# Kernel optimization log

Measured on AMD Instinct MI355X. Metric: run time of the kernel, lower is better.

## Reference

```python
import jax, jax.numpy as jnp
import numpy as np

NUM_HEADS = 16
HEAD_DIM = 64
HIDDEN = NUM_HEADS * HEAD_DIM
LN_EPS = 1e-6


def setup_inputs() -> dict:
    key = jax.random.key(0)
    ks = jax.random.split(key, 5)
    B, T, H = 2, 2048, HIDDEN
    s = 1.0 / np.sqrt(H)
    return {
        "h": jax.random.normal(ks[0], (B, T, H), jnp.float32),
        "Wq": jax.random.normal(ks[1], (H, H), jnp.float32) * s,
        "bq": jnp.zeros((H,), jnp.float32),
        "Wk": jax.random.normal(ks[2], (H, H), jnp.float32) * s,
        "bk": jnp.zeros((H,), jnp.float32),
        "Wv": jax.random.normal(ks[3], (H, H), jnp.float32) * s,
        "bv": jnp.zeros((H,), jnp.float32),
        "Wo": jax.random.normal(ks[4], (H, H), jnp.float32) * s,
        "bo": jnp.zeros((H,), jnp.float32),
        "gamma": jnp.ones((H,), jnp.float32),
        "beta": jnp.zeros((H,), jnp.float32),
    }


def _split_heads(x):
    B, T, H = x.shape
    return x.reshape(B, T, NUM_HEADS, HEAD_DIM).transpose(0, 2, 1, 3)  # [B,h,T,d]


def reference(h, Wq, bq, Wk, bk, Wv, bv, Wo, bo, gamma, beta):
    # QKV projections (nn.Linear: x @ W^T + b)
    Q = _split_heads(h @ Wq.T + bq)
    K = _split_heads(h @ Wk.T + bk)
    V = _split_heads(h @ Wv.T + bv)
    scale = HEAD_DIM ** -0.5
    scores = jnp.einsum("bhqd,bhkd->bhqk", Q, K) * scale  # [B,h,T,T]
    attn = jax.nn.softmax(scores, axis=-1)
    ctx = jnp.einsum("bhqk,bhkd->bhqd", attn, V)          # [B,h,T,d]
    B, _, T, _ = ctx.shape
    ctx = ctx.transpose(0, 2, 1, 3).reshape(B, T, HIDDEN)
    out = ctx @ Wo.T + bo + h  # dropout is identity at eval
    # LayerNorm(eps=1e-6)
    mu = out.mean(-1, keepdims=True)
    var = jnp.mean((out - mu) ** 2, -1, keepdims=True)
    return (out - mu) * jax.lax.rsqrt(var + LN_EPS) * gamma + beta
```

## Files before the change

kernel.cpp:

```cpp
#include <hip/hip_runtime.h>
#include <hip/hip_bf16.h>

#define NH   16
#define HD   64
#define HID  1024
#define TSEQ 2048
#define BATCH 2
#define KSCALE 0.18033688011112042f

typedef __attribute__((ext_vector_type(4))) float f32x4;
typedef __attribute__((ext_vector_type(8))) short s16x8;
typedef __attribute__((ext_vector_type(4))) short s16x4;
typedef __attribute__((ext_vector_type(8))) _Float16 f16x8;
typedef __attribute__((ext_vector_type(4))) _Float16 f16x4;

__device__ __forceinline__ unsigned short f2bf(float f) {
  union { float f; unsigned int u; } v; v.f = f;
  unsigned int r = v.u + 0x7fffu + ((v.u >> 16) & 1u);
  return (unsigned short)(r >> 16);
}
__device__ __forceinline__ float bf2f(unsigned short b) {
  union { unsigned int u; float f; } v; v.u = ((unsigned int)b) << 16; return v.f;
}

__device__ __forceinline__ void async_cp16(const unsigned short* g, unsigned short* l) {
  __builtin_amdgcn_global_load_lds(
      (const __attribute__((address_space(1))) unsigned int*)g,
      (__attribute__((address_space(3))) unsigned int*)l, 16, 0, 0);
}

__global__ __launch_bounds__(256) void cast_all_k(
    const float* __restrict__ h,
    const float* __restrict__ w0, const float* __restrict__ w1,
    const float* __restrict__ w2, const float* __restrict__ w3,
    unsigned short* __restrict__ hb, unsigned short* __restrict__ wbase) {
  int i = blockIdx.x * 256 + threadIdx.x;
  const float* src; unsigned short* dst; int idx; float sc = 1.f;
  if (i < 1048576) { src = h; dst = hb; idx = i; }
  else {
    int idx4 = i - 1048576;
    int w = idx4 >> 18;
    idx = idx4 & 262143;
    src = (w == 0) ? w0 : (w == 1) ? w1 : (w == 2) ? w2 : w3;
    dst = wbase + (size_t)(idx4 - idx) * 4;
    if (w == 1) sc = KSCALE;
  }
  float4 v = ((const float4*)src)[idx];
  ushort4 o;
  o.x = f2bf(v.x * sc); o.y = f2bf(v.y * sc); o.z = f2bf(v.z * sc); o.w = f2bf(v.w * sc);
  ((ushort4*)dst)[idx] = o;
}

__device__ __forceinline__ void gemm_core(const unsigned short* __restrict__ Ag,
                                          const unsigned short* __restrict__ Bg,
                                          unsigned short* Ash, unsigned short* Bsh,
                                          f32x4 acc[4][4]) {
  const int tid  = threadIdx.x;
  const int lane = tid & 63;
  const int wave = tid >> 6;
  const int l15  = lane & 15;
  const int quad = lane >> 4;
  const int wm   = (wave >> 1) * 64;
  const int wn   = (wave & 1) * 64;
  const int idx0 = tid * 8;
  const int idx1 = idx0 + 2048;
  const int r0 = idx0 >> 5, c0 = idx0 & 31;
  const int r1 = idx1 >> 5, c1 = idx1 & 31;
#pragma unroll
  for (int i = 0; i < 4; ++i)
#pragma unroll
    for (int j = 0; j < 4; ++j) acc[i][j] = f32x4{0.f, 0.f, 0.f, 0.f};

  for (int k0 = 0; k0 < HID; k0 += 32) {
    __syncthreads();
    async_cp16(Ag + r0 * HID + k0 + c0, Ash + idx0);
    async_cp16(Ag + r1 * HID + k0 + c1, Ash + idx1);
    async_cp16(Bg + r0 * HID + k0 + c0, Bsh + idx0);
    async_cp16(Bg + r1 * HID + k0 + c1, Bsh + idx1);
    __syncthreads();
    s16x8 af[4], bfr[4];
#pragma unroll
    for (int i = 0; i < 4; ++i)
      af[i] = *(const s16x8*)(Ash + (wm + i * 16 + l15) * 32 + quad * 8);
#pragma unroll
    for (int j = 0; j < 4; ++j)
      bfr[j] = *(const s16x8*)(Bsh + (wn + j * 16 + l15) * 32 + quad * 8);
#pragma unroll
    for (int i = 0; i < 4; ++i)
#pragma unroll
      for (int j = 0; j < 4; ++j)
        acc[i][j] = __builtin_amdgcn_mfma_f32_16x16x32_bf16(af[i], bfr[j], acc[i][j], 0, 0, 0);
  }
}

__global__ __launch_bounds__(256) void gemm_qkv(
    const unsigned short* __restrict__ hb,
    const unsigned short* __restrict__ wq, const unsigned short* __restrict__ wk,
    const unsigned short* __restrict__ wv,
    const float* __restrict__ bq, const float* __restrict__ bk, const float* __restrict__ bv,
    unsigned short* __restrict__ qo, unsigned short* __restrict__ ko,
    unsigned short* __restrict__ vto) {
  __shared__ unsigned short Ash[128 * 32];
  __shared__ unsigned short Bsh[128 * 32];
  const unsigned short* Bw; const float* bias; float bsc = 1.f;
  if (blockIdx.z == 0)      { Bw = wq; bias = bq; }
  else if (blockIdx.z == 1) { Bw = wk; bias = bk; bsc = KSCALE; }
  else                      { Bw = wv; bias = bv; }
  const int bm = blockIdx.y * 128, bn = blockIdx.x * 128;
  f32x4 acc[4][4];
  gemm_core(hb + (size_t)bm * HID, Bw + (size_t)bn * HID, Ash, Bsh, acc);

  const int tid = threadIdx.x, lane = tid & 63, wave = tid >> 6;
  const int l15 = lane & 15, quad = lane >> 4;
  const int wm = (wave >> 1) * 64, wn = (wave & 1) * 64;
  if (blockIdx.z == 2) {
#pragma unroll
    for (int j = 0; j < 4; ++j) {
      const int col = bn + wn + j * 16 + l15;
      const float bb = bias[col];
      const int head = col >> 6, d = col & 63;
#pragma unroll
      for (int i = 0; i < 4; ++i) {
        const int row0 = bm + wm + i * 16 + quad * 4;
        const int bI = row0 >> 11, t0 = row0 & 2047;
        unsigned short o[4];
#pragma unroll
        for (int r = 0; r < 4; ++r) {
          _Float16 hv = (_Float16)(acc[i][j][r] + bb);
          o[r] = __builtin_bit_cast(unsigned short, hv);
        }
        *(s16x4*)(vto + ((size_t)((bI * NH + head) * HD + d)) * TSEQ + t0) = *(const s16x4*)o;
      }
    }
  } else {
    unsigned short* outp = (blockIdx.z == 0) ? qo : ko;
#pragma unroll
    for (int j = 0; j < 4; ++j) {
      const int col = bn + wn + j * 16 + l15;
      const float bb = bias[col] * bsc;
      const int head = col >> 6, d = col & 63;
#pragma unroll
      for (int i = 0; i < 4; ++i) {
#pragma unroll
        for (int r = 0; r < 4; ++r) {
          const int row = bm + wm + i * 16 + quad * 4 + r;
          const int bI = row >> 11, t = row & 2047;
          outp[(((size_t)(bI * NH + head) * TSEQ) + t) * HD + d] = f2bf(acc[i][j][r] + bb);
        }
      }
    }
  }
}

__global__ __launch_bounds__(256) void gemm_out(
    const unsigned short* __restrict__ ctx, const unsigned short* __restrict__ wo,
    const float* __restrict__ bo, const float* __restrict__ hres,
    float* __restrict__ outf) {
  __shared__ unsigned short Ash[128 * 32];
  __shared__ unsigned short Bsh[64 * 32];
  const int tid = threadIdx.x, lane = tid & 63, wave = tid >> 6;
  const int l15 = lane & 15, quad = lane >> 4;
  const int wm = (wave >> 1) * 64, wn = (wave & 1) * 32;
  const int bm = blockIdx.y * 128, bn = blockIdx.x * 64;
  const unsigned short* Ag = ctx + (size_t)bm * HID;
  const unsigned short* Bg = wo + (size_t)bn * HID;
  const int idx0 = tid * 8, idx1 = idx0 + 2048;
  const int r0 = idx0 >> 5, c0 = idx0 & 31;
  const int r1 = idx1 >> 5, c1 = idx1 & 31;
  f32x4 acc[4][2];
#pragma unroll
  for (int i = 0; i < 4; ++i)
#pragma unroll
    for (int j = 0; j < 2; ++j) acc[i][j] = f32x4{0.f, 0.f, 0.f, 0.f};

  for (int k0 = 0; k0 < HID; k0 += 32) {
    __syncthreads();
    async_cp16(Ag + r0 * HID + k0 + c0, Ash + idx0);
    async_cp16(Ag + r1 * HID + k0 + c1, Ash + idx1);
    async_cp16(Bg + r0 * HID + k0 + c0, Bsh + idx0);
    __syncthreads();
    s16x8 af[4], bfr[2];
#pragma unroll
    for (int i = 0; i < 4; ++i)
      af[i] = *(const s16x8*)(Ash + (wm + i * 16 + l15) * 32 + quad * 8);
#pragma unroll
    for (int j = 0; j < 2; ++j)
      bfr[j] = *(const s16x8*)(Bsh + (wn + j * 16 + l15) * 32 + quad * 8);
#pragma unroll
    for (int i = 0; i < 4; ++i)
#pragma unroll
      for (int j = 0; j < 2; ++j)
        acc[i][j] = __builtin_amdgcn_mfma_f32_16x16x32_bf16(af[i], bfr[j], acc[i][j], 0, 0, 0);
  }
#pragma unroll
  for (int j = 0; j < 2; ++j) {
    const int col = bn + wn + j * 16 + l15;
    const float bb = bo[col];
#pragma unroll
    for (int i = 0; i < 4; ++i) {
#pragma unroll
      for (int r = 0; r < 4; ++r) {
        const int row = bm + wm + i * 16 + quad * 4 + r;
        const size_t off = (size_t)row * HID + col;
        outf[off] = acc[i][j][r] + bb + hres[off];
      }
    }
  }
}

__global__ __launch_bounds__(256, 2) void attn_k(
    const unsigned short* __restrict__ qb, const unsigned short* __restrict__ kb,
    const unsigned short* __restrict__ vt, unsigned short* __restrict__ ctx,
    unsigned short* __restrict__ Opart, float* __restrict__ rsumP,
    int split, int ntiles) {
  __shared__ unsigned short Ksh[64 * 72];
  __shared__ unsigned short Vsh[64 * 72];

  const int tid = threadIdx.x, lane = tid & 63, wave = tid >> 6;
  const int l15 = lane & 15, quad = lane >> 4;
  const int z = blockIdx.z;
  const int b = split ? (z >> 1) : z;
  const int half = split ? (z & 1) : 0;
  const int h = blockIdx.y, qt = blockIdx.x;
  const size_t ho = ((size_t)(b * NH + h)) * TSEQ * HD;
  const unsigned short* Qh = qb + ho;
  const unsigned short* Kh = kb + ho;
  const unsigned short* Vh = vt + ho;
  const int q0 = qt * 128 + wave * 32;
  const int kt0 = half * ntiles;

  s16x8 qf[2][2];
#pragma unroll
  for (int s = 0; s < 2; ++s)
#pragma unroll
    for (int ks = 0; ks < 2; ++ks)
      qf[s][ks] = *(const s16x8*)(Qh + (size_t)(q0 + s * 16 + l15) * HD + ks * 32 + quad * 8);

  f32x4 accO[4][2];
  float rsum[2];
#pragma unroll
  for (int n2 = 0; n2 < 4; ++n2)
#pragma unroll
    for (int s = 0; s < 2; ++s) accO[n2][s] = f32x4{0.f, 0.f, 0.f, 0.f};
  rsum[0] = rsum[1] = 0.f;

  const int sr = tid >> 3, sc = (tid & 7) * 8;
  s16x8 kreg[2], vreg[2];
#pragma unroll
  for (int hf = 0; hf < 2; ++hf) {
    kreg[hf] = *(const s16x8*)(Kh + (size_t)(kt0 * 64 + sr + hf * 32) * HD + sc);
    vreg[hf] = *(const s16x8*)(Vh + (size_t)(sr + hf * 32) * TSEQ + kt0 * 64 + sc);
  }

  for (int kt = 0; kt < ntiles; ++kt) {
    __syncthreads();
#pragma unroll
    for (int hf = 0; hf < 2; ++hf) {
      *(s16x8*)(Ksh + (sr + hf * 32) * 72 + sc) = kreg[hf];
      *(s16x8*)(Vsh + (sr + hf * 32) * 72 + sc) = vreg[hf];
    }
    __syncthreads();
    if (kt + 1 < ntiles) {
      const int k0n = (kt0 + kt + 1) * 64;
#pragma unroll
      for (int hf = 0; hf < 2; ++hf) {
        kreg[hf] = *(const s16x8*)(Kh + (size_t)(k0n + sr + hf * 32) * HD + sc);
        vreg[hf] = *(const s16x8*)(Vh + (size_t)(sr + hf * 32) * TSEQ + k0n + sc);
      }
    }

    f32x4 accS[2][4];
#pragma unroll
    for (int s = 0; s < 2; ++s)
#pragma unroll
      for (int n = 0; n < 4; ++n) accS[s][n] = f32x4{0.f, 0.f, 0.f, 0.f};
#pragma unroll
    for (int ks = 0; ks < 2; ++ks) {
#pragma unroll
      for (int n = 0; n < 4; ++n) {
        s16x8 kf = *(const s16x8*)(Ksh + (n * 16 + l15) * 72 + ks * 32 + quad * 8);
#pragma unroll
        for (int s = 0; s < 2; ++s)
          accS[s][n] = __builtin_amdgcn_mfma_f32_16x16x32_bf16(kf, qf[s][ks], accS[s][n], 0, 0, 0);
      }
    }

    f16x4 pB[2][4];
#pragma unroll
    for (int s = 0; s < 2; ++s)
#pragma unroll
      for (int n = 0; n < 4; ++n) {
        float e0 = exp2f(accS[s][n][0]);
        float e1 = exp2f(accS[s][n][1]);
        float e2 = exp2f(accS[s][n][2]);
        float e3 = exp2f(accS[s][n][3]);
        rsum[s] += (e0 + e1) + (e2 + e3);
        pB[s][n] = f16x4{(_Float16)e0, (_Float16)e1, (_Float16)e2, (_Float16)e3};
      }

#pragma unroll
    for (int n = 0; n < 4; ++n) {
#pragma unroll
      for (int n2 = 0; n2 < 4; ++n2) {
        f16x4 vA = *(const f16x4*)(Vsh + (n2 * 16 + l15) * 72 + n * 16 + quad * 4);
#pragma unroll
        for (int s = 0; s < 2; ++s)
          accO[n2][s] = __builtin_amdgcn_mfma_f32_16x16x16f16(vA, pB[s][n], accO[n2][s], 0, 0, 0);
      }
    }
  }

#pragma unroll
  for (int s = 0; s < 2; ++s) {
    float t = rsum[s];
    t += __shfl_xor(t, 16, 64);
    t += __shfl_xor(t, 32, 64);
    rsum[s] = t;
  }

  if (split) {
    const size_t ob = ((size_t)((half * BATCH + b) * NH + h)) * TSEQ * HD;
#pragma unroll
    for (int s = 0; s < 2; ++s) {
      const int t = q0 + s * 16 + l15;
#pragma unroll
      for (int n2 = 0; n2 < 4; ++n2) {
        const int d0 = n2 * 16 + quad * 4;
        unsigned short o[4];
#pragma unroll
        for (int r = 0; r < 4; ++r) o[r] = f2bf(accO[n2][s][r]);
        *(s16x4*)(Opart + ob + (size_t)t * HD + d0) = *(const s16x4*)o;
      }
    }
    if (quad == 0) {
      const size_t rb = ((size_t)((half * BATCH + b) * NH + h)) * TSEQ;
#pragma unroll
      for (int s = 0; s < 2; ++s)
        rsumP[rb + q0 + s * 16 + l15] = rsum[s];
    }
  } else {
#pragma unroll
    for (int s = 0; s < 2; ++s) {
      const int t = q0 + s * 16 + l15;
      const float inv = 1.f / rsum[s];
#pragma unroll
      for (int n2 = 0; n2 < 4; ++n2) {
        const int d0 = n2 * 16 + quad * 4;
        unsigned short o[4];
#pragma unroll
        for (int r = 0; r < 4; ++r) o[r] = f2bf(accO[n2][s][r] * inv);
        *(s16x4*)(ctx + ((size_t)(b * TSEQ + t)) * HID + h * HD + d0) = *(const s16x4*)o;
      }
    }
  }
}

__global__ __launch_bounds__(256) void combine_k(
    const unsigned short* __restrict__ Opart, const float* __restrict__ rsumP,
    unsigned short* __restrict__ ctx) {
  const int gtid = blockIdx.x * 256 + threadIdx.x;
  const int d = (gtid & 7) * 8;
  const int rem = gtid >> 3;
  const int t = rem & 2047;
  const int bh = rem >> 11;
  const size_t offA = ((size_t)bh * TSEQ + t) * HD + d;
  const size_t offB = ((size_t)(32 + bh) * TSEQ + t) * HD + d;
  s16x8 a = *(const s16x8*)(Opart + offA);
  s16x8 c = *(const s16x8*)(Opart + offB);
  const float ra = rsumP[(size_t)bh * TSEQ + t];
  const float rb = rsumP[(size_t)(32 + bh) * TSEQ + t];
  const float inv = 1.f / (ra + rb);
  unsigned short o[8];
#pragma unroll
  for (int j = 0; j < 8; ++j)
    o[j] = f2bf((bf2f(((const unsigned short*)&a)[j]) + bf2f(((const unsigned short*)&c)[j])) * inv);
  const int b = bh >> 4, h = bh & 15;
  *(s16x8*)(ctx + ((size_t)(b * TSEQ + t)) * HID + h * HD + d) = *(const s16x8*)o;
}

__global__ __launch_bounds__(256) void ln_k(float* __restrict__ io,
                                            const float* __restrict__ gamma,
                                            const float* __restrict__ beta) {
  const int row = blockIdx.x, tid = threadIdx.x;
  float x[4]; float s = 0.f, s2 = 0.f;
#pragma unroll
  for (int i = 0; i < 4; ++i) {
    x[i] = io[(size_t)row * HID + tid + i * 256];
    s += x[i]; s2 += x[i] * x[i];
  }
#pragma unroll
  for (int off = 1; off < 64; off <<= 1) {
    s  += __shfl_xor(s, off, 64);
    s2 += __shfl_xor(s2, off, 64);
  }
  __shared__ float red[8];
  const int wave = tid >> 6;
  if ((tid & 63) == 0) { red[wave] = s; red[wave + 4] = s2; }
  __syncthreads();
  s  = red[0] + red[1] + red[2] + red[3];
  s2 = red[4] + red[5] + red[6] + red[7];
  const float mean = s * (1.f / HID);
  const float var  = s2 * (1.f / HID) - mean * mean;
  const float rstd = rsqrtf(var + 1e-6f);
#pragma unroll
  for (int i = 0; i < 4; ++i) {
    const int col = tid + i * 256;
    io[(size_t)row * HID + col] = (x[i] - mean) * rstd * gamma[col] + beta[col];
  }
}

extern "C" void kernel_launch(void* const* d_in, const int* in_sizes, int n_in,
                              void* d_out, int out_size, void* d_ws, size_t ws_size,
                              hipStream_t stream) {
  const float* h    = (const float*)d_in[0];
  const float* Wq   = (const float*)d_in[1];
  const float* bq   = (const float*)d_in[2];
  const float* Wk   = (const float*)d_in[3];
  const float* bk   = (const float*)d_in[4];
  const float* Wv   = (const float*)d_in[5];
  const float* bv   = (const float*)d_in[6];
  const float* Wo   = (const float*)d_in[7];
  const float* bo   = (const float*)d_in[8];
  const float* gamma = (const float*)d_in[9];
  const float* beta  = (const float*)d_in[10];
  float* out = (float*)d_out;

  unsigned short* hb   = (unsigned short*)d_ws;
  unsigned short* wqb  = hb  + 4194304;
  unsigned short* wkb  = wqb + 1048576;
  unsigned short* wvb  = wkb + 1048576;
  unsigned short* wob  = wvb + 1048576;
  unsigned short* qb   = wob + 1048576;
  unsigned short* kb   = qb  + 4194304;
  unsigned short* vtf  = kb  + 4194304;
  unsigned short* Opart = vtf + 4194304;
  float*          rsumP = (float*)(Opart + 8388608);
  unsigned short* ctxb = hb;

  const size_t need = (size_t)(28 * 1024 * 1024) * 2 + 131072 * 4;
  const int split = (ws_size >= need) ? 1 : 0;

  cast_all_k<<<8192, 256, 0, stream>>>(h, Wq, Wk, Wv, Wo, hb, wqb);
  gemm_qkv<<<dim3(8, 32, 3), 256, 0, stream>>>(hb, wqb, wkb, wvb, bq, bk, bv, qb, kb, vtf);
  if (split) {
    attn_k<<<dim3(TSEQ / 128, NH, BATCH * 2), 256, 0, stream>>>(qb, kb, vtf, ctxb, Opart, rsumP, 1, 16);
    combine_k<<<2048, 256, 0, stream>>>(Opart, rsumP, ctxb);
  } else {
    attn_k<<<dim3(TSEQ / 128, NH, BATCH), 256, 0, stream>>>(qb, kb, vtf, ctxb, Opart, rsumP, 0, 32);
  }
  gemm_out<<<dim3(16, 32), 256, 0, stream>>>(ctxb, wob, bo, h, out);
  ln_k<<<4096, 256, 0, stream>>>(out, gamma, beta);
}
```

Before: 238.0 us.

## Generalize attention split-K to four key partitions and use packed f16 conversion

Result: slower. 244.3 us (+2.7%).

```diff
diff --git a/kernel.cpp b/kernel.cpp
--- a/kernel.cpp
+++ b/kernel.cpp
@@ -13,6 +13,7 @@
 typedef __attribute__((ext_vector_type(4))) short s16x4;
 typedef __attribute__((ext_vector_type(8))) _Float16 f16x8;
 typedef __attribute__((ext_vector_type(4))) _Float16 f16x4;
+typedef __attribute__((ext_vector_type(2))) _Float16 f16x2;
 
 __device__ __forceinline__ unsigned short f2bf(float f) {
   union { float f; unsigned int u; } v; v.f = f;
@@ -212,22 +213,22 @@
     const unsigned short* __restrict__ qb, const unsigned short* __restrict__ kb,
     const unsigned short* __restrict__ vt, unsigned short* __restrict__ ctx,
     unsigned short* __restrict__ Opart, float* __restrict__ rsumP,
-    int split, int ntiles) {
+    int lsplit, int ntiles) {
   __shared__ unsigned short Ksh[64 * 72];
   __shared__ unsigned short Vsh[64 * 72];
 
   const int tid = threadIdx.x, lane = tid & 63, wave = tid >> 6;
   const int l15 = lane & 15, quad = lane >> 4;
   const int z = blockIdx.z;
-  const int b = split ? (z >> 1) : z;
-  const int half = split ? (z & 1) : 0;
+  const int b = z >> lsplit;
+  const int part = z & ((1 << lsplit) - 1);
   const int h = blockIdx.y, qt = blockIdx.x;
   const size_t ho = ((size_t)(b * NH + h)) * TSEQ * HD;
   const unsigned short* Qh = qb + ho;
   const unsigned short* Kh = kb + ho;
   const unsigned short* Vh = vt + ho;
   const int q0 = qt * 128 + wave * 32;
-  const int kt0 = half * ntiles;
+  const int kt0 = part * ntiles;
 
   s16x8 qf[2][2];
 #pragma unroll
@@ -295,7 +296,9 @@
         float e2 = exp2f(accS[s][n][2]);
         float e3 = exp2f(accS[s][n][3]);
         rsum[s] += (e0 + e1) + (e2 + e3);
-        pB[s][n] = f16x4{(_Float16)e0, (_Float16)e1, (_Float16)e2, (_Float16)e3};
+        f16x2 lo = __builtin_bit_cast(f16x2, __builtin_amdgcn_cvt_pkrtz(e0, e1));
+        f16x2 hi = __builtin_bit_cast(f16x2, __builtin_amdgcn_cvt_pkrtz(e2, e3));
+        pB[s][n] = f16x4{lo[0], lo[1], hi[0], hi[1]};
       }
 
 #pragma unroll
@@ -318,8 +321,9 @@
     rsum[s] = t;
   }
 
-  if (split) {
-    const size_t ob = ((size_t)((half * BATCH + b) * NH + h)) * TSEQ * HD;
+  if (lsplit) {
+    const int slot = (part * BATCH + b) * NH + h;
+    const size_t ob = (size_t)slot * TSEQ * HD;
 #pragma unroll
     for (int s = 0; s < 2; ++s) {
       const int t = q0 + s * 16 + l15;
@@ -333,7 +337,7 @@
       }
     }
     if (quad == 0) {
-      const size_t rb = ((size_t)((half * BATCH + b) * NH + h)) * TSEQ;
+      const size_t rb = (size_t)slot * TSEQ;
 #pragma unroll
       for (int s = 0; s < 2; ++s)
         rsumP[rb + q0 + s * 16 + l15] = rsum[s];
@@ -357,23 +361,25 @@
 
 __global__ __launch_bounds__(256) void combine_k(
     const unsigned short* __restrict__ Opart, const float* __restrict__ rsumP,
-    unsigned short* __restrict__ ctx) {
+    unsigned short* __restrict__ ctx, int nparts) {
   const int gtid = blockIdx.x * 256 + threadIdx.x;
   const int d = (gtid & 7) * 8;
   const int rem = gtid >> 3;
   const int t = rem & 2047;
   const int bh = rem >> 11;
-  const size_t offA = ((size_t)bh * TSEQ + t) * HD + d;
-  const size_t offB = ((size_t)(32 + bh) * TSEQ + t) * HD + d;
-  s16x8 a = *(const s16x8*)(Opart + offA);
-  s16x8 c = *(const s16x8*)(Opart + offB);
-  const float ra = rsumP[(size_t)bh * TSEQ + t];
-  const float rb = rsumP[(size_t)(32 + bh) * TSEQ + t];
-  const float inv = 1.f / (ra + rb);
+  float acc[8] = {0, 0, 0, 0, 0, 0, 0, 0};
+  float rs = 0.f;
+  for (int p = 0; p < nparts; ++p) {
+    const int slot = p * 32 + bh;
+    s16x8 a = *(const s16x8*)(Opart + ((size_t)slot * TSEQ + t) * HD + d);
+#pragma unroll
+    for (int j = 0; j < 8; ++j) acc[j] += bf2f(((const unsigned short*)&a)[j]);
+    rs += rsumP[(size_t)slot * TSEQ + t];
+  }
+  const float inv = 1.f / rs;
   unsigned short o[8];
 #pragma unroll
-  for (int j = 0; j < 8; ++j)
-    o[j] = f2bf((bf2f(((const unsigned short*)&a)[j]) + bf2f(((const unsigned short*)&c)[j])) * inv);
+  for (int j = 0; j < 8; ++j) o[j] = f2bf(acc[j] * inv);
   const int b = bh >> 4, h = bh & 15;
   *(s16x8*)(ctx + ((size_t)(b * TSEQ + t)) * HID + h * HD + d) = *(const s16x8*)o;
 }
@@ -434,20 +440,21 @@
   unsigned short* kb   = qb  + 4194304;
   unsigned short* vtf  = kb  + 4194304;
   unsigned short* Opart = vtf + 4194304;
-  float*          rsumP = (float*)(Opart + 8388608);
   unsigned short* ctxb = hb;
 
-  const size_t need = (size_t)(28 * 1024 * 1024) * 2 + 131072 * 4;
-  const int split = (ws_size >= need) ? 1 : 0;
+  const size_t base = (size_t)(vtf + 4194304 - hb) * 2;
+  int lsplit = 0;
+  if (ws_size >= base + 4u * 8388608 + 4u * 262144) lsplit = 2;
+  else if (ws_size >= base + 2u * 8388608 + 2u * 262144) lsplit = 1;
+  const int nparts = 1 << lsplit;
+  float* rsumP = (float*)(Opart + (size_t)nparts * 4194304);
 
   cast_all_k<<<8192, 256, 0, stream>>>(h, Wq, Wk, Wv, Wo, hb, wqb);
   gemm_qkv<<<dim3(8, 32, 3), 256, 0, stream>>>(hb, wqb, wkb, wvb, bq, bk, bv, qb, kb, vtf);
-  if (split) {
-    attn_k<<<dim3(TSEQ / 128, NH, BATCH * 2), 256, 0, stream>>>(qb, kb, vtf, ctxb, Opart, rsumP, 1, 16);
-    combine_k<<<2048, 256, 0, stream>>>(Opart, rsumP, ctxb);
-  } else {
-    attn_k<<<dim3(TSEQ / 128, NH, BATCH), 256, 0, stream>>>(qb, kb, vtf, ctxb, Opart, rsumP, 0, 32);
-  }
+  attn_k<<<dim3(TSEQ / 128, NH, BATCH << lsplit), 256, 0, stream>>>(
+      qb, kb, vtf, ctxb, Opart, rsumP, lsplit, 32 >> lsplit);
+  if (lsplit)
+    combine_k<<<2048, 256, 0, stream>>>(Opart, rsumP, ctxb, nparts);
   gemm_out<<<dim3(16, 32), 256, 0, stream>>>(ctxb, wob, bo, h, out);
   ln_k<<<4096, 256, 0, stream>>>(out, gamma, beta);
 }
```
